# Performance work log

Measured on AMD Instinct MI355X. Metric: run time of the kernel, lower is better.

The kernel has to match this reference:

```python
import jax, jax.numpy as jnp
import numpy as np

B, C, H, W = 32, 64, 56, 56
REPN, NK, SMALL = 50, 17, 3   # repN=64-int(64*0.23), nk=ceil(51/3)
GROUPS = 4                     # N_rep
EPS = 1e-5


def _build_index_mats():
    """Reduce the fallback's python scatter-add loops to exact linear maps.
    For flat position p=r*NK+j the roll shifts depend only on p%3, so each
    shift class s gets a (REPN,NK) count matrix over source nk-slots."""
    rng = np.random.RandomState(123)
    ghost = np.sort(rng.choice(C, C - REPN, replace=False))
    rep = np.array(sorted(set(range(C)) - set(ghost.tolist())), np.int32)
    Mh = np.zeros((3, REPN, NK), np.int32)
    Mv = np.zeros((3, REPN, NK), np.int32)
    Mid = np.zeros((REPN, NK), np.int32)
    for _ in range(GROUPS):
        for r in range(REPN):
            perm = rng.permutation(NK)
            for p in range(NK):
                Mh[(r * NK + p) % 3, r, perm[p]] += 1
        for r in range(REPN):
            perm = rng.permutation(NK)
            for p in range(NK):
                Mv[(r * NK + p) % 3, r, perm[p]] += 1
        kk = rng.randint(0, NK, REPN)
        for r in range(REPN):
            Mid[r, kk[r]] += 1
    return ghost.astype(np.int32), rep, Mh, Mv, Mid


def setup_inputs() -> dict:
    key = jax.random.key(0)
    k1, k2, k3 = jax.random.split(key, 3)
    ghost, rep, Mh, Mv, Mid = _build_index_mats()
    return {
        "inputs": jax.random.normal(k1, (B, C, H, W), jnp.float32),
        "w0": jax.random.normal(k2, (REPN * NK, 1, SMALL, SMALL), jnp.float32) * 0.1,
        "w1": jax.random.normal(k3, (REPN * NK, 1, SMALL, SMALL), jnp.float32) * 0.1,
        "Mh": jnp.asarray(Mh), "Mv": jnp.asarray(Mv), "Mid": jnp.asarray(Mid),
        "ghost_idx": jnp.asarray(ghost), "rep_idx": jnp.asarray(rep),
    }


def _bn(x):
    # BatchNorm2d in training mode, affine weight=1 / bias=0 (init values)
    m = x.mean(axis=(0, 2, 3), keepdims=True)
    v = x.var(axis=(0, 2, 3), keepdims=True)
    return (x - m) / jnp.sqrt(v + EPS)


def reference(inputs, w0, w1, Mh, Mv, Mid, ghost_idx, rep_idx):
    rep_in = inputs[:, rep_idx]      # (B, REPN, H, W)
    ghost_in = inputs[:, ghost_idx]  # (B, ghostN, H, W)

    def conv(w):  # depthwise-grouped conv: groups=REPN, each 1->NK channels
        return jax.lax.conv_general_dilated(
            rep_in, w, window_strides=(1, 1), padding=((2, 2), (2, 2)),
            dimension_numbers=('NCHW', 'OIHW', 'NCHW'),
            feature_group_count=REPN)

    out = conv(w0) + conv(w1)                       # (B, REPN*NK, H+2, W+2)
    xv = out.reshape(B, REPN, NK, H + 2, W + 2)

    Mhf, Mvf, Midf = (m.astype(xv.dtype) for m in (Mh, Mv, Mid))
    sh1, sw1 = (0, 1, 2), (0, 2, 1)   # lora1: shifts (i%3, 2i%3)
    sh2, sw2 = (0, 2, 1), (0, 1, 2)   # lora2: shifts (2i%3, i%3)

    lora1 = sum(jnp.roll(jnp.einsum('rk,brkhw->brhw', Mhf[s], xv),
                         (sh1[s], sw1[s]), axis=(2, 3)) for s in range(3))
    lora2 = sum(jnp.roll(jnp.einsum('rk,brkhw->brhw', Mvf[s], xv),
                         (sh2[s], sw2[s]), axis=(2, 3)) for s in range(3))
    small = jnp.einsum('rk,brkhw->brhw', Midf, xv)

    # center-crop back to (H, W): dh = dw = 1
    lora1 = lora1[:, :, 1:1 + H, 1:1 + W]
    lora2 = lora2[:, :, 1:1 + H, 1:1 + W]
    small = small[:, :, 1:1 + H, 1:1 + W]

    x = _bn(lora1) + _bn(lora2) + _bn(small) + rep_in
    return jnp.concatenate([x, ghost_in], axis=1)   # (B, C, H, W)
```

## Files before the change

### kernel.cpp

```cpp
#include <hip/hip_runtime.h>

#define Bn 32
#define Cn 64
#define Hn 56
#define Wn 56
#define REPN 50
#define NKn 17
#define HWn (Hn*Wn)
#define NSTATf 100352.0f
#define EPSf 1e-5f

#define PLANE (Bn*REPN*HWn)
#define L1_OFF 0
#define L2_OFF PLANE
#define SM_OFF (2*PLANE)
#define PART_OFF (3*PLANE)
#define WEFF_OFF (3*PLANE + 9600)

#define SEGH 7
#define SEGS 8
#define NTASK (SEGS*14)

__global__ void k_weff(const float* __restrict__ w0, const float* __restrict__ w1,
                       const int* __restrict__ Mh, const int* __restrict__ Mv,
                       const int* __restrict__ Mid, float* __restrict__ ws)
{
    int idx = blockIdx.x * blockDim.x + threadIdx.x;
    if (idx >= REPN*63) return;
    int r   = idx / 63;
    int rem = idx % 63;
    int t   = rem / 9;
    int ij  = rem % 9;
    const int* M = (t < 3) ? (Mh + (t*REPN + r)*NKn)
                 : (t < 6) ? (Mv + ((t-3)*REPN + r)*NKn)
                           : (Mid + r*NKn);
    float acc = 0.f;
    #pragma unroll
    for (int k = 0; k < NKn; ++k)
        acc += (float)M[k] * (w0[(r*NKn + k)*9 + ij] + w1[(r*NKn + k)*9 + ij]);
    ws[WEFF_OFF + idx] = acc;
}

__device__ __forceinline__ void load_row8c(const float* __restrict__ ch, int row, int q,
                                           float* __restrict__ X, float& c55)
{
    bool rv = (row >= 0) && (row < Hn);
    int rc = rv ? row : 0;
    const float* rp = ch + rc*Wn;
    float4 c0 = *(const float4*)(rp + (q ? 4*q - 4 : 0));
    float4 c1 = *(const float4*)(rp + 4*q);
    int ox = (4*q + 4 <= 55) ? 4*q + 4 : 55;
    float cx = rp[ox];
    float mr = rv ? 1.f : 0.f;
    float m0 = (rv && q > 0)  ? 1.f : 0.f;
    float mx = (rv && q < 13) ? 1.f : 0.f;
    X[0]=c0.y*m0; X[1]=c0.z*m0; X[2]=c0.w*m0;
    X[3]=c1.x*mr; X[4]=c1.y*mr; X[5]=c1.z*mr; X[6]=c1.w*mr;
    X[7]=cx*mx;
    c55 = (q == 0) ? rp[55]*mr : 0.f;
}

__global__ void __launch_bounds__(128) k_conv(const float* __restrict__ in,
        const int* __restrict__ rep_idx, float* __restrict__ ws)
{
    int bid = blockIdx.x;
    int r = bid % REPN;
    int b = bid / REPN;
    int tid = threadIdx.x;

    const float* wr = ws + WEFF_OFF + r*63;
    float wk[63];
    #pragma unroll
    for (int i = 0; i < 63; ++i) wk[i] = wr[i];

    int cin = rep_idx[r];
    const float* ch = in + ((size_t)(b*Cn + cin))*HWn;

    float s1=0.f,q1=0.f,s2=0.f,q2=0.f,s3=0.f,q3=0.f;

    if (tid < NTASK) {
        int seg = tid / 14;
        int q   = tid - seg*14;
        int h0  = seg * SEGH;
        bool top = (seg == 0);

        float W[5][8], C[5], T[8];
        {
            float dummy;
            if (top) load_row8c(ch, 55, q, T, dummy);
        }
        #pragma unroll
        for (int k = 0; k < 5; ++k)
            load_row8c(ch, h0 - 3 + k, q, W[k], C[k]);

        size_t base = ((size_t)(b*REPN + r))*HWn;
        float* p1 = ws + L1_OFF + base;
        float* p2 = ws + L2_OFF + base;
        float* p3 = ws + SM_OFF + base;

        #pragma unroll
        for (int s = 0; s < SEGH; ++s) {
            int h = h0 + s;
            float Wn8[8], Cn1;
            load_row8c(ch, h + 2, q, Wn8, Cn1);

            float l1[4], l2[4], sm[4];
            #pragma unroll
            for (int p = 0; p < 4; ++p) { l1[p]=0.f; l2[p]=0.f; sm[p]=0.f; }
            #pragma unroll
            for (int i = 0; i < 3; ++i)
                #pragma unroll
                for (int j = 0; j < 3; ++j) {
                    float wh0 = wk[i*3+j],    wv0 = wk[27+i*3+j], wid = wk[54+i*3+j];
                    float wh1 = wk[9+i*3+j],  wv2 = wk[45+i*3+j];
                    float wh2 = wk[18+i*3+j], wv1 = wk[36+i*3+j];
                    #pragma unroll
                    for (int p = 0; p < 4; ++p) {
                        float a  = W[2+i][p+2+j];
                        l1[p] = fmaf(a, wh0, l1[p]);
                        l2[p] = fmaf(a, wv0, l2[p]);
                        sm[p] = fmaf(a, wid, sm[p]);
                        float bA = W[1+i][p+j];
                        l1[p] = fmaf(bA, wh1, l1[p]);
                        l2[p] = fmaf(bA, wv2, l2[p]);
                        float bB = W[i][p+1+j];
                        l1[p] = fmaf(bB, wh2, l1[p]);
                        l2[p] = fmaf(bB, wv1, l2[p]);
                    }
                }
            if (q == 0) {
                #pragma unroll
                for (int i = 0; i < 3; ++i) {
                    l1[0] = fmaf(C[1+i], wk[9+3*i],  l1[0]);
                    l2[0] = fmaf(C[1+i], wk[45+3*i], l2[0]);
                }
            }
            if (s == 0 && top) {
                #pragma unroll
                for (int j = 0; j < 3; ++j)
                    #pragma unroll
                    for (int p = 0; p < 4; ++p) {
                        l1[p] = fmaf(T[p+1+j], wk[18+j], l1[p]);
                        l2[p] = fmaf(T[p+1+j], wk[36+j], l2[p]);
                    }
            }
            int o = h*Wn + 4*q;
            *(float4*)(p1 + o) = make_float4(l1[0],l1[1],l1[2],l1[3]);
            *(float4*)(p2 + o) = make_float4(l2[0],l2[1],l2[2],l2[3]);
            *(float4*)(p3 + o) = make_float4(sm[0],sm[1],sm[2],sm[3]);
            #pragma unroll
            for (int p = 0; p < 4; ++p) {
                s1 += l1[p]; q1 += l1[p]*l1[p];
                s2 += l2[p]; q2 += l2[p]*l2[p];
                s3 += sm[p]; q3 += sm[p]*sm[p];
            }
            #pragma unroll
            for (int k = 0; k < 4; ++k) {
                #pragma unroll
                for (int x = 0; x < 8; ++x) W[k][x] = W[k+1][x];
                C[k] = C[k+1];
            }
            #pragma unroll
            for (int x = 0; x < 8; ++x) W[4][x] = Wn8[x];
            C[4] = Cn1;
        }
    }

    __shared__ float red[2][6];
    float vals[6] = {s1,q1,s2,q2,s3,q3};
    int lane = tid & 63, wave = tid >> 6;
    #pragma unroll
    for (int v = 0; v < 6; ++v) {
        float x = vals[v];
        for (int o = 32; o; o >>= 1) x += __shfl_down(x, o, 64);
        if (lane == 0) red[wave][v] = x;
    }
    __syncthreads();
    if (tid < 6)
        ws[PART_OFF + (tid*REPN + r)*Bn + b] = red[0][tid] + red[1][tid];
}

__global__ void __launch_bounds__(256) k_final(const float* __restrict__ in,
        const int* __restrict__ rep_idx, const int* __restrict__ ghost_idx,
        const float* __restrict__ ws, float* __restrict__ out)
{
    int bid = blockIdx.x;
    int c = bid % Cn;
    int b = bid / Cn;
    int tid = threadIdx.x;

    if (c >= REPN) {
        int cin = ghost_idx[c - REPN];
        const float4* s4 = (const float4*)(in + ((size_t)(b*Cn + cin))*HWn);
        float4* d4 = (float4*)(out + ((size_t)(b*Cn + c))*HWn);
        for (int i = tid; i < HWn/4; i += 256) d4[i] = s4[i];
        return;
    }

    __shared__ float sred[6];
    int r = c;
    if (tid < 6) {
        const float* pp = ws + PART_OFF + (tid*REPN + r)*Bn;
        float s = 0.f;
        #pragma unroll
        for (int i = 0; i < Bn; ++i) s += pp[i];
        sred[tid] = s;
    }
    __syncthreads();
    const float inv = 1.0f / NSTATf;
    float m1 = sred[0]*inv, v1 = sred[1]*inv - m1*m1;
    float m2 = sred[2]*inv, v2 = sred[3]*inv - m2*m2;
    float m3 = sred[4]*inv, v3 = sred[5]*inv - m3*m3;
    float r1 = rsqrtf(v1 + EPSf), r2 = rsqrtf(v2 + EPSf), r3 = rsqrtf(v3 + EPSf);

    int cin = rep_idx[r];
    size_t base = (size_t)(b*REPN + r)*HWn;
    const float4* p1 = (const float4*)(ws + L1_OFF + base);
    const float4* p2 = (const float4*)(ws + L2_OFF + base);
    const float4* p3 = (const float4*)(ws + SM_OFF + base);
    const float4* rin = (const float4*)(in + ((size_t)(b*Cn + cin))*HWn);
    float4* d4 = (float4*)(out + ((size_t)(b*Cn + c))*HWn);

    for (int i = tid; i < HWn/4; i += 256) {
        float4 a = p1[i], d = p2[i], e = p3[i], x = rin[i];
        float4 o;
        o.x = (a.x-m1)*r1 + (d.x-m2)*r2 + (e.x-m3)*r3 + x.x;
        o.y = (a.y-m1)*r1 + (d.y-m2)*r2 + (e.y-m3)*r3 + x.y;
        o.z = (a.z-m1)*r1 + (d.z-m2)*r2 + (e.z-m3)*r3 + x.z;
        o.w = (a.w-m1)*r1 + (d.w-m2)*r2 + (e.w-m3)*r3 + x.w;
        d4[i] = o;
    }
}

extern "C" void kernel_launch(void* const* d_in, const int* in_sizes, int n_in,
                              void* d_out, int out_size, void* d_ws, size_t ws_size,
                              hipStream_t stream) {
    const float* in   = (const float*)d_in[0];
    const float* w0   = (const float*)d_in[1];
    const float* w1   = (const float*)d_in[2];
    const int*   Mh   = (const int*)d_in[3];
    const int*   Mv   = (const int*)d_in[4];
    const int*   Mid  = (const int*)d_in[5];
    const int*   ghost= (const int*)d_in[6];
    const int*   rep  = (const int*)d_in[7];
    float* out  = (float*)d_out;
    float* ws   = (float*)d_ws;

    k_weff<<<(REPN*63 + 255)/256, 256, 0, stream>>>(w0, w1, Mh, Mv, Mid, ws);
    k_conv<<<Bn*REPN, 128, 0, stream>>>(in, rep, ws);
    k_final<<<Bn*Cn, 256, 0, stream>>>(in, rep, ghost, ws, out);
}
```

Baseline: 125.0 us.

## Recompute depthwise conv in output pass instead of storing intermediate planes

The stencil computation moves into a shared templated walker that is called twice. A stats kernel runs it to produce the BN partial sums only, and the output kernel recomputes the convolution and applies normalization plus the residual directly. This removes writing and re-reading three full-size intermediate planes in the workspace, trading that memory traffic for a second pass of conv arithmetic and a second read of the input. Block sizes of the output and weight kernels change to 128 threads, and the residual now comes from registers already loaded for the stencil.

Result: no change. 124.7 us (-0.2%).

```diff
diff --git a/kernel.cpp b/kernel.cpp
--- a/kernel.cpp
+++ b/kernel.cpp
@@ -10,16 +10,11 @@
 #define NSTATf 100352.0f
 #define EPSf 1e-5f
 
-#define PLANE (Bn*REPN*HWn)
-#define L1_OFF 0
-#define L2_OFF PLANE
-#define SM_OFF (2*PLANE)
-#define PART_OFF (3*PLANE)
-#define WEFF_OFF (3*PLANE + 9600)
+#define PART_OFF 0
+#define WEFF_OFF 9600
 
 #define SEGH 7
-#define SEGS 8
-#define NTASK (SEGS*14)
+#define NTASK 112
 
 __global__ void k_weff(const float* __restrict__ w0, const float* __restrict__ w1,
                        const int* __restrict__ Mh, const int* __restrict__ Mv,
@@ -60,7 +55,87 @@
     c55 = (q == 0) ? rp[55]*mr : 0.f;
 }
 
-__global__ void __launch_bounds__(128) k_conv(const float* __restrict__ in,
+template <typename F>
+__device__ __forceinline__ void conv_walk(const float* __restrict__ ch,
+        const float (&wk)[63], int tid, F emit)
+{
+    if (tid >= NTASK) return;
+    int seg = tid / 14;
+    int q   = tid - seg*14;
+    int h0  = seg * SEGH;
+    bool top = (seg == 0);
+
+    float W[5][8], C[5], T[8];
+    {
+        float dummy;
+        if (top) load_row8c(ch, 55, q, T, dummy);
+    }
+    #pragma unroll
+    for (int k = 0; k < 5; ++k)
+        load_row8c(ch, h0 - 3 + k, q, W[k], C[k]);
+
+    #pragma unroll
+    for (int s = 0; s < SEGH; ++s) {
+        int h = h0 + s;
+        float Wn8[8], Cn1;
+        load_row8c(ch, h + 2, q, Wn8, Cn1);
+
+        float l1[4], l2[4], sm[4];
+        #pragma unroll
+        for (int p = 0; p < 4; ++p) { l1[p]=0.f; l2[p]=0.f; sm[p]=0.f; }
+        #pragma unroll
+        for (int i = 0; i < 3; ++i)
+            #pragma unroll
+            for (int j = 0; j < 3; ++j) {
+                float wh0 = wk[i*3+j],    wv0 = wk[27+i*3+j], wid = wk[54+i*3+j];
+                float wh1 = wk[9+i*3+j],  wv2 = wk[45+i*3+j];
+                float wh2 = wk[18+i*3+j], wv1 = wk[36+i*3+j];
+                #pragma unroll
+                for (int p = 0; p < 4; ++p) {
+                    float a  = W[2+i][p+2+j];
+                    l1[p] = fmaf(a, wh0, l1[p]);
+                    l2[p] = fmaf(a, wv0, l2[p]);
+                    sm[p] = fmaf(a, wid, sm[p]);
+                    float bA = W[1+i][p+j];
+                    l1[p] = fmaf(bA, wh1, l1[p]);
+                    l2[p] = fmaf(bA, wv2, l2[p]);
+                    float bB = W[i][p+1+j];
+                    l1[p] = fmaf(bB, wh2, l1[p]);
+                    l2[p] = fmaf(bB, wv1, l2[p]);
+                }
+            }
+        if (q == 0) {
+            #pragma unroll
+            for (int i = 0; i < 3; ++i) {
+                l1[0] = fmaf(C[1+i], wk[9+3*i],  l1[0]);
+                l2[0] = fmaf(C[1+i], wk[45+3*i], l2[0]);
+            }
+        }
+        if (s == 0 && top) {
+            #pragma unroll
+            for (int j = 0; j < 3; ++j)
+                #pragma unroll
+                for (int p = 0; p < 4; ++p) {
+                    l1[p] = fmaf(T[p+1+j], wk[18+j], l1[p]);
+                    l2[p] = fmaf(T[p+1+j], wk[36+j], l2[p]);
+                }
+        }
+        float res[4] = {W[3][3], W[3][4], W[3][5], W[3][6]};
+        emit(h, q, l1, l2, sm, res);
+
+        #pragma unroll
+        for (int k = 0; k < 4; ++k) {
+            #pragma unroll
+            for (int x = 0; x < 8; ++x) W[k][x] = W[k+1][x];
+            C[k] = C[k+1];
+        }
+        #pragma unroll
+        for (int x = 0; x < 8; ++x) W[4][x] = Wn8[x];
+        C[4] = Cn1;
+    }
+}
+
+__global__ void __launch_bounds__(128) k_stats(const float* __restrict__ in,
         const int* __restrict__ rep_idx, float* __restrict__ ws)
 {
     int bid = blockIdx.x;
@@ -77,94 +152,16 @@
     const float* ch = in + ((size_t)(b*Cn + cin))*HWn;
 
     float s1=0.f,q1=0.f,s2=0.f,q2=0.f,s3=0.f,q3=0.f;
-
-    if (tid < NTASK) {
-        int seg = tid / 14;
-        int q   = tid - seg*14;
-        int h0  = seg * SEGH;
-        bool top = (seg == 0);
-
-        float W[5][8], C[5], T[8];
-        {
-            float dummy;
-            if (top) load_row8c(ch, 55, q, T, dummy);
-        }
-        #pragma unroll
-        for (int k = 0; k < 5; ++k)
-            load_row8c(ch, h0 - 3 + k, q, W[k], C[k]);
-
-        size_t base = ((size_t)(b*REPN + r))*HWn;
-        float* p1 = ws + L1_OFF + base;
-        float* p2 = ws + L2_OFF + base;
-        float* p3 = ws + SM_OFF + base;
-
-        #pragma unroll
-        for (int s = 0; s < SEGH; ++s) {
-            int h = h0 + s;
-            float Wn8[8], Cn1;
-            load_row8c(ch, h + 2, q, Wn8, Cn1);
-
-            float l1[4], l2[4], sm[4];
-            #pragma unroll
-            for (int p = 0; p < 4; ++p) { l1[p]=0.f; l2[p]=0.f; sm[p]=0.f; }
-            #pragma unroll
-            for (int i = 0; i < 3; ++i)
-                #pragma unroll
-                for (int j = 0; j < 3; ++j) {
-                    float wh0 = wk[i*3+j],    wv0 = wk[27+i*3+j], wid = wk[54+i*3+j];
-                    float wh1 = wk[9+i*3+j],  wv2 = wk[45+i*3+j];
-                    float wh2 = wk[18+i*3+j], wv1 = wk[36+i*3+j];
-                    #pragma unroll
-                    for (int p = 0; p < 4; ++p) {
-                        float a  = W[2+i][p+2+j];
-                        l1[p] = fmaf(a, wh0, l1[p]);
-                        l2[p] = fmaf(a, wv0, l2[p]);
-                        sm[p] = fmaf(a, wid, sm[p]);
-                        float bA = W[1+i][p+j];
-                        l1[p] = fmaf(bA, wh1, l1[p]);
-                        l2[p] = fmaf(bA, wv2, l2[p]);
-                        float bB = W[i][p+1+j];
-                        l1[p] = fmaf(bB, wh2, l1[p]);
-                        l2[p] = fmaf(bB, wv1, l2[p]);
-                    }
-                }
-            if (q == 0) {
-                #pragma unroll
-                for (int i = 0; i < 3; ++i) {
-                    l1[0] = fmaf(C[1+i], wk[9+3*i],  l1[0]);
-                    l2[0] = fmaf(C[1+i], wk[45+3*i], l2[0]);
-                }
-            }
-            if (s == 0 && top) {
-                #pragma unroll
-                for (int j = 0; j < 3; ++j)
-                    #pragma unroll
-                    for (int p = 0; p < 4; ++p) {
-                        l1[p] = fmaf(T[p+1+j], wk[18+j], l1[p]);
-                        l2[p] = fmaf(T[p+1+j], wk[36+j], l2[p]);
-                    }
-            }
-            int o = h*Wn + 4*q;
-            *(float4*)(p1 + o) = make_float4(l1[0],l1[1],l1[2],l1[3]);
-            *(float4*)(p2 + o) = make_float4(l2[0],l2[1],l2[2],l2[3]);
-            *(float4*)(p3 + o) = make_float4(sm[0],sm[1],sm[2],sm[3]);
+    conv_walk(ch, wk, tid,
+        [&](int h, int q, float* l1, float* l2, float* sm, float* res) {
+            (void)h; (void)q; (void)res;
             #pragma unroll
             for (int p = 0; p < 4; ++p) {
                 s1 += l1[p]; q1 += l1[p]*l1[p];
                 s2 += l2[p]; q2 += l2[p]*l2[p];
                 s3 += sm[p]; q3 += sm[p]*sm[p];
             }
-            #pragma unroll
-            for (int k = 0; k < 4; ++k) {
-                #pragma unroll
-                for (int x = 0; x < 8; ++x) W[k][x] = W[k+1][x];
-                C[k] = C[k+1];
-            }
-            #pragma unroll
-            for (int x = 0; x < 8; ++x) W[4][x] = Wn8[x];
-            C[4] = Cn1;
-        }
-    }
+        });
 
     __shared__ float red[2][6];
     float vals[6] = {s1,q1,s2,q2,s3,q3};
@@ -180,7 +177,7 @@
         ws[PART_OFF + (tid*REPN + r)*Bn + b] = red[0][tid] + red[1][tid];
 }
 
-__global__ void __launch_bounds__(256) k_final(const float* __restrict__ in,
+__global__ void __launch_bounds__(128) k_out(const float* __restrict__ in,
         const int* __restrict__ rep_idx, const int* __restrict__ ghost_idx,
         const float* __restrict__ ws, float* __restrict__ out)
 {
@@ -193,12 +190,12 @@
         int cin = ghost_idx[c - REPN];
         const float4* s4 = (const float4*)(in + ((size_t)(b*Cn + cin))*HWn);
         float4* d4 = (float4*)(out + ((size_t)(b*Cn + c))*HWn);
-        for (int i = tid; i < HWn/4; i += 256) d4[i] = s4[i];
+        for (int i = tid; i < HWn/4; i += 128) d4[i] = s4[i];
         return;
     }
 
+    int r = c;
     __shared__ float sred[6];
-    int r = c;
     if (tid < 6) {
         const float* pp = ws + PART_OFF + (tid*REPN + r)*Bn;
         float s = 0.f;
@@ -213,23 +210,24 @@
     float m3 = sred[4]*inv, v3 = sred[5]*inv - m3*m3;
     float r1 = rsqrtf(v1 + EPSf), r2 = rsqrtf(v2 + EPSf), r3 = rsqrtf(v3 + EPSf);
 
+    const float* wr = ws + WEFF_OFF + r*63;
+    float wk[63];
+    #pragma unroll
+    for (int i = 0; i < 63; ++i) wk[i] = wr[i];
+
     int cin = rep_idx[r];
-    size_t base = (size_t)(b*REPN + r)*HWn;
-    const float4* p1 = (const float4*)(ws + L1_OFF + base);
-    const float4* p2 = (const float4*)(ws + L2_OFF + base);
-    const float4* p3 = (const float4*)(ws + SM_OFF + base);
-    const float4* rin = (const float4*)(in + ((size_t)(b*Cn + cin))*HWn);
-    float4* d4 = (float4*)(out + ((size_t)(b*Cn + c))*HWn);
-
-    for (int i = tid; i < HWn/4; i += 256) {
-        float4 a = p1[i], d = p2[i], e = p3[i], x = rin[i];
-        float4 o;
-        o.x = (a.x-m1)*r1 + (d.x-m2)*r2 + (e.x-m3)*r3 + x.x;
-        o.y = (a.y-m1)*r1 + (d.y-m2)*r2 + (e.y-m3)*r3 + x.y;
-        o.z = (a.z-m1)*r1 + (d.z-m2)*r2 + (e.z-m3)*r3 + x.z;
-        o.w = (a.w-m1)*r1 + (d.w-m2)*r2 + (e.w-m3)*r3 + x.w;
-        d4[i] = o;
-    }
+    const float* ch = in + ((size_t)(b*Cn + cin))*HWn;
+    float* dst = out + ((size_t)(b*Cn + c))*HWn;
+
+    conv_walk(ch, wk, tid,
+        [&](int h, int q, float* l1, float* l2, float* sm, float* res) {
+            float4 o;
+            o.x = (l1[0]-m1)*r1 + (l2[0]-m2)*r2 + (sm[0]-m3)*r3 + res[0];
+            o.y = (l1[1]-m1)*r1 + (l2[1]-m2)*r2 + (sm[1]-m3)*r3 + res[1];
+            o.z = (l1[2]-m1)*r1 + (l2[2]-m2)*r2 + (sm[2]-m3)*r3 + res[2];
+            o.w = (l1[3]-m1)*r1 + (l2[3]-m2)*r2 + (sm[3]-m3)*r3 + res[3];
+            *(float4*)(dst + h*Wn + 4*q) = o;
+        });
 }
 
 extern "C" void kernel_launch(void* const* d_in, const int* in_sizes, int n_in,
@@ -246,7 +244,7 @@
     float* out  = (float*)d_out;
     float* ws   = (float*)d_ws;
 
-    k_weff<<<(REPN*63 + 255)/256, 256, 0, stream>>>(w0, w1, Mh, Mv, Mid, ws);
-    k_conv<<<Bn*REPN, 128, 0, stream>>>(in, rep, ws);
-    k_final<<<Bn*Cn, 256, 0, stream>>>(in, rep, ghost, ws, out);
-}
+    k_weff<<<(REPN*63 + 127)/128, 128, 0, stream>>>(w0, w1, Mh, Mv, Mid, ws);
+    k_stats<<<Bn*REPN, 128, 0, stream>>>(in, rep, ws);
+    k_out<<<Bn*Cn, 128, 0, stream>>>(in, rep, ghost, ws, out);
+}
```
